# Kernel optimization log

Hardware: AMD Instinct MI355X
Metric: run time of the kernel (lower is better)

## Reference

```python
import jax, jax.numpy as jnp
import numpy as np

N = 8192       # num_nodes
F_IN = 128     # num_features
H = 32         # hidden_dim
C = 10         # num_classes
E = 262144     # num_edges (avg degree 32)
EPS = 1e-5     # BatchNorm1d eps


def setup_inputs() -> dict:
    key = jax.random.key(0)
    ks = jax.random.split(key, 24)
    rn = lambda k, shape, s=0.05: jax.random.normal(k, shape, jnp.float32) * s
    z = lambda n: jnp.zeros((n,), jnp.float32)
    return {
        "b": jax.random.normal(ks[0], (N, N), jnp.float32),
        "x": jax.random.normal(ks[1], (N, F_IN), jnp.float32),
        "edge_index": jax.random.randint(ks[2], (2, E), 0, N, jnp.int32),
        # GCNConv weights (stored [in,out]) + biases
        "W0": rn(ks[3], (F_IN, H)), "bc0": z(H),
        "W1": rn(ks[4], (H, H)),    "bc1": z(H),
        # BatchNorm affine params
        "g0": jnp.ones((H,), jnp.float32), "be0": z(H),
        "g1": jnp.ones((H,), jnp.float32), "be1": z(H),
        # autoencoder Linears (stored [in,out])
        "Wa0": rn(ks[5], (N, H)), "ba0": z(H),
        "Wa1": rn(ks[6], (H, H)), "ba1": z(H),
        "Wa2": rn(ks[7], (H, H)), "ba2": z(H),
        "Wa3": rn(ks[8], (H, N)), "ba3": z(N),
        # jump classifier: Linear(num_layers*H, C)
        "Wj": rn(ks[9], (2 * H, C)), "bj": z(C),
    }


def _gcn_conv(x, W, bias, src, dst):
    # PyG GCNConv: D^{-1/2}(A+I)D^{-1/2} X W + bias (src/dst already include self-loops)
    h = x @ W                                             # [N, out]
    deg = jax.ops.segment_sum(jnp.ones(src.shape[0], h.dtype), dst, num_segments=N)
    dinv = jax.lax.rsqrt(deg)                             # deg >= 1 due to self-loops
    norm = dinv[src] * dinv[dst]                          # [E+N]
    agg = jax.ops.segment_sum(norm[:, None] * h[src], dst, num_segments=N)
    return agg + bias


def _bn(x, g, b):
    # BatchNorm1d in training mode: batch stats over node dim, biased variance
    m = jnp.mean(x, axis=0)
    v = jnp.var(x, axis=0)
    return g * (x - m) * jax.lax.rsqrt(v + EPS) + b


def reference(b, x, edge_index, W0, bc0, W1, bc1, g0, be0, g1, be1,
              Wa0, ba0, Wa1, ba1, Wa2, ba2, Wa3, ba3, Wj, bj):
    loop = jnp.arange(N, dtype=edge_index.dtype)
    src = jnp.concatenate([edge_index[0], loop])
    dst = jnp.concatenate([edge_index[1], loop])

    # layer 0
    h = jax.nn.relu(_bn(_gcn_conv(x, W0, bc0, src, dst), g0, be0))
    x0 = h
    b = b @ Wa0 + ba0          # [N, H]
    h = h + b
    # layer 1
    h = jax.nn.relu(_bn(_gcn_conv(h, W1, bc1, src, dst), g1, be1))
    x1 = h
    b = b @ Wa1 + ba1
    # (torch computes x = x1 + b here, but it is dead after the last layer)
    # decoder tail: autoencoder[2], autoencoder[3]
    b = b @ Wa2 + ba2
    b = b @ Wa3 + ba3          # [N, N]

    out = jnp.concatenate([x0, x1], axis=1) @ Wj + bj
    return jax.nn.log_softmax(out, axis=-1), b
```

## Files before the change

### kernel.cpp

```cpp
#include <hip/hip_runtime.h>
#include <math.h>

#define NN 8192
#define FIN 128
#define HD 32
#define NC 10
#define NE 262144
#define EPSBN 1e-5f

typedef short short8 __attribute__((ext_vector_type(8)));
typedef float f32x4 __attribute__((ext_vector_type(4)));

__device__ __forceinline__ float bf2f(unsigned short b) {
  unsigned int u = ((unsigned int)b) << 16;
  float f;
  __builtin_memcpy(&f, &u, 4);
  return f;
}
__device__ __forceinline__ unsigned short f2bf(float f) {
  unsigned int u;
  __builtin_memcpy(&u, &f, 4);
  u = u + 0x7fffu + ((u >> 16) & 1u);
  return (unsigned short)(u >> 16);
}
__device__ __forceinline__ short8 ld_bf8(const unsigned short* p) {
  uint4 u = *(const uint4*)p;
  return __builtin_bit_cast(short8, u);
}
__device__ __forceinline__ float ldin(const void* p, int i, int isf) {
  if (isf) return ((const float*)p)[i];
  return bf2f(((const unsigned short*)p)[i]);
}

__global__ void detect_k(const void* __restrict__ b, int* __restrict__ flag) {
  const unsigned short* p = (const unsigned short*)b;
  int t = threadIdx.x;
  unsigned short s = p[2 * t];
  int e = (s >> 7) & 0xFF;
  int hit = (e >= 110 && e <= 135) ? 1 : 0;
  __shared__ int cnt[256];
  cnt[t] = hit;
  __syncthreads();
  for (int o = 128; o > 0; o >>= 1) {
    if (t < o) cnt[t] += cnt[t + o];
    __syncthreads();
  }
  if (t == 0) flag[0] = (cnt[0] < 128) ? 1 : 0;
}

__global__ void prep_T(const void* __restrict__ Wa1, const void* __restrict__ ba1,
                       const void* __restrict__ Wa2, const void* __restrict__ ba2,
                       const int* __restrict__ flg, float* __restrict__ T, float* __restrict__ vv) {
  int isf = *flg;
  __shared__ float sW1[1024], sW2[1024];
  int t = threadIdx.x;
  sW1[t] = ldin(Wa1, t, isf);
  sW2[t] = ldin(Wa2, t, isf);
  __syncthreads();
  {
    int c = t >> 5, c2 = t & 31;
    float acc = 0.f;
    for (int k = 0; k < 32; k++) acc += sW1[c * 32 + k] * sW2[k * 32 + c2];
    T[c * 32 + c2] = acc;
  }
  if (t < 32) {
    float acc = ldin(ba2, t, isf);
    for (int k = 0; k < 32; k++) acc += ldin(ba1, k, isf) * sW2[k * 32 + t];
    vv[t] = acc;
  }
}

__global__ void compute_Rp(const void* __restrict__ Wa3, const void* __restrict__ ba3,
                           const float* __restrict__ T, const float* __restrict__ vv,
                           const int* __restrict__ flg,
                           float* __restrict__ r2, unsigned short* __restrict__ Rp) {
  int isf = *flg;
  __shared__ float sT[1024], sv[32];
  int t = threadIdx.x;
  for (int i = t; i < 1024; i += 256) sT[i] = T[i];
  if (t < 32) sv[t] = vv[t];
  __syncthreads();
  int j = blockIdx.x * 256 + t;
  float w3[32];
  for (int c = 0; c < 32; c++) w3[c] = ldin(Wa3, c * NN + j, isf);
  float rr = ldin(ba3, j, isf);
  for (int c = 0; c < 32; c++) rr += sv[c] * w3[c];
  r2[j] = rr;
  float Rcol[32];
  for (int c = 0; c < 32; c++) {
    float acc = 0.f;
    for (int cp = 0; cp < 32; cp++) acc += sT[c * 32 + cp] * w3[cp];
    Rcol[c] = acc;
  }
  int jt = j >> 4, n = j & 15;
  for (int q = 0; q < 4; q++)
    for (int jj = 0; jj < 8; jj++)
      Rp[(size_t)(jt * 64 + q * 16 + n) * 8 + jj] = f2bf(Rcol[q * 8 + jj]);
}

__global__ void pack_Bp(const void* __restrict__ Wa0, const int* __restrict__ flg,
                        unsigned short* __restrict__ Bp) {
  int isf = *flg;
  int tid = blockIdx.x * 256 + threadIdx.x;
  int kb = tid >> 7;
  int h = (tid >> 6) & 1;
  int L = tid & 63;
  int q = L >> 4, n = L & 15;
  int base_k = kb * 32 + q * 8;
  if (isf) {
    const float* W = (const float*)Wa0;
    for (int j = 0; j < 8; j++)
      Bp[(size_t)((kb * 2 + h) * 64 + L) * 8 + j] = f2bf(W[(base_k + j) * HD + h * 16 + n]);
  } else {
    const unsigned short* W = (const unsigned short*)Wa0;
    for (int j = 0; j < 8; j++)
      Bp[(size_t)((kb * 2 + h) * 64 + L) * 8 + j] = W[(base_k + j) * HD + h * 16 + n];
  }
}

__global__ void deg_k(const int* __restrict__ dst, float* __restrict__ deg) {
  int e = blockIdx.x * 256 + threadIdx.x;
  atomicAdd(&deg[dst[e]], 1.0f);
}
__global__ void dinv_k(float* __restrict__ deg) {
  int i = blockIdx.x * 256 + threadIdx.x;
  deg[i] = rsqrtf(deg[i] + 1.0f);
}

__global__ void gemm_x_w0(const void* __restrict__ x, const void* __restrict__ W0,
                          const int* __restrict__ flg, float* __restrict__ h0) {
  int isf = *flg;
  __shared__ float sW[FIN * HD];
  __shared__ float sx[8 * FIN];
  int t = threadIdx.x;
  for (int i = t; i < FIN * HD; i += 256) sW[i] = ldin(W0, i, isf);
  int row0 = blockIdx.x * 8;
  for (int i = t; i < 8 * FIN; i += 256) {
    int r = i >> 7, k = i & 127;
    sx[i] = ldin(x, (row0 + r) * FIN + k, isf);
  }
  __syncthreads();
  int r = t >> 5, c = t & 31;
  float acc = 0.f;
  for (int k = 0; k < FIN; k++) acc += sx[r * FIN + k] * sW[k * HD + c];
  h0[(row0 + r) * HD + c] = acc;
}

__global__ void scatter_agg(const int* __restrict__ src, const int* __restrict__ dst,
                            const float* __restrict__ dinv, const float* __restrict__ h,
                            float* __restrict__ agg) {
  int tid = blockIdx.x * 256 + threadIdx.x;
  int idx = tid >> 5, c = tid & 31;
  int s, d;
  if (idx < NE) { s = src[idx]; d = dst[idx]; }
  else { s = d = idx - NE; }
  float wgt = dinv[s] * dinv[d];
  atomicAdd(&agg[d * HD + c], wgt * h[s * HD + c]);
}

__global__ void bn_stats(const float* __restrict__ xin, float* __restrict__ sum, float* __restrict__ sq) {
  int t = threadIdx.x;
  int c = t & 31;
  int g = t >> 5;
  float s = 0.f, q = 0.f;
  for (int r = blockIdx.x * 8 + g; r < NN; r += 2048) {
    float v = xin[r * HD + c];
    s += v;
    q += v * v;
  }
  __shared__ float ss[256], qq[256];
  ss[t] = s; qq[t] = q;
  __syncthreads();
  if (t < 128) { ss[t] += ss[t + 128]; qq[t] += qq[t + 128]; }
  __syncthreads();
  if (t < 64) { ss[t] += ss[t + 64]; qq[t] += qq[t + 64]; }
  __syncthreads();
  if (t < 32) {
    atomicAdd(&sum[c], ss[t] + ss[t + 32]);
    atomicAdd(&sq[c], qq[t] + qq[t + 32]);
  }
}

__global__ void bn_coef(const float* __restrict__ sum, const float* __restrict__ sq,
                        const void* __restrict__ g, const void* __restrict__ be,
                        const int* __restrict__ flg, float* __restrict__ a, float* __restrict__ bb) {
  int isf = *flg;
  int c = threadIdx.x;
  if (c < 32) {
    float m = sum[c] * (1.0f / 8192.0f);
    float var = fmaxf(sq[c] * (1.0f / 8192.0f) - m * m, 0.0f);
    float rstd = rsqrtf(var + EPSBN);
    float ac = ldin(g, c, isf) * rstd;
    a[c] = ac;
    bb[c] = ldin(be, c, isf) - m * ac;
  }
}

__global__ void gemm_b_wa0(const void* __restrict__ Bm, const unsigned short* __restrict__ Bp,
                           const int* __restrict__ flg, float* __restrict__ b1) {
  int isf = *flg;
  int t = threadIdx.x;
  int w = (blockIdx.x << 2) + (t >> 6);
  int L = t & 63;
  int rt = w >> 3, kq = w & 7;
  int q = L >> 4, n = L & 15;
  size_t aoff = (size_t)(rt * 16 + n) * NN + kq * 1024 + q * 8;
  f32x4 acc0 = {0.f, 0.f, 0.f, 0.f};
  f32x4 acc1 = {0.f, 0.f, 0.f, 0.f};
  int kb0 = kq * 32;
  if (isf) {
    const float* arow = (const float*)Bm + aoff;
    for (int i = 0; i < 32; i++) {
      f32x4 u0 = *(const f32x4*)(arow + i * 32);
      f32x4 u1 = *(const f32x4*)(arow + i * 32 + 4);
      union { unsigned short s[8]; short8 v; } au;
      au.s[0] = f2bf(u0[0]); au.s[1] = f2bf(u0[1]); au.s[2] = f2bf(u0[2]); au.s[3] = f2bf(u0[3]);
      au.s[4] = f2bf(u1[0]); au.s[5] = f2bf(u1[1]); au.s[6] = f2bf(u1[2]); au.s[7] = f2bf(u1[3]);
      const unsigned short* bpp = Bp + (size_t)((kb0 + i) * 2) * 512 + L * 8;
      acc0 = __builtin_amdgcn_mfma_f32_16x16x32_bf16(au.v, ld_bf8(bpp), acc0, 0, 0, 0);
      acc1 = __builtin_amdgcn_mfma_f32_16x16x32_bf16(au.v, ld_bf8(bpp + 512), acc1, 0, 0, 0);
    }
  } else {
    const unsigned short* arow = (const unsigned short*)Bm + aoff;
    for (int i = 0; i < 32; i++) {
      short8 a = ld_bf8(arow + i * 32);
      const unsigned short* bpp = Bp + (size_t)((kb0 + i) * 2) * 512 + L * 8;
      acc0 = __builtin_amdgcn_mfma_f32_16x16x32_bf16(a, ld_bf8(bpp), acc0, 0, 0, 0);
      acc1 = __builtin_amdgcn_mfma_f32_16x16x32_bf16(a, ld_bf8(bpp + 512), acc1, 0, 0, 0);
    }
  }
  int orow = rt * 16 + q * 4;
  for (int r = 0; r < 4; r++) {
    atomicAdd(&b1[(orow + r) * HD + n], acc0[r]);
    atomicAdd(&b1[(orow + r) * HD + n + 16], acc1[r]);
  }
}

__global__ void fuse0(float* __restrict__ aggA, const float* __restrict__ b1,
                      const void* __restrict__ ba0, const float* __restrict__ a,
                      const float* __restrict__ bb, const int* __restrict__ flg,
                      float* __restrict__ x0) {
  int isf = *flg;
  int i = blockIdx.x * 256 + threadIdx.x;
  int c = i & 31;
  float xv = fmaxf(a[c] * aggA[i] + bb[c], 0.0f);
  x0[i] = xv;
  aggA[i] = xv + b1[i] + ldin(ba0, c, isf);
}

__global__ void gemm_h_w1(float* __restrict__ hbuf, const void* __restrict__ W1,
                          const int* __restrict__ flg) {
  int isf = *flg;
  __shared__ float sW[1024], sh[256];
  int t = threadIdx.x;
  for (int i = t; i < 1024; i += 256) sW[i] = ldin(W1, i, isf);
  int row0 = blockIdx.x * 8;
  {
    int r = t >> 5, k = t & 31;
    sh[t] = hbuf[(row0 + r) * HD + k];
  }
  __syncthreads();
  int r = t >> 5, c = t & 31;
  float acc = 0.f;
  for (int k = 0; k < 32; k++) acc += sh[r * 32 + k] * sW[k * HD + c];
  hbuf[(row0 + r) * HD + c] = acc;
}

__global__ void bn_relu(float* __restrict__ agg, const float* __restrict__ a,
                        const float* __restrict__ bb) {
  int i = blockIdx.x * 256 + threadIdx.x;
  int c = i & 31;
  agg[i] = fmaxf(a[c] * agg[i] + bb[c], 0.0f);
}

__global__ void classifier(const float* __restrict__ x0, const float* __restrict__ x1,
                           const void* __restrict__ Wj, const void* __restrict__ bj,
                           const int* __restrict__ flg, void* __restrict__ outv) {
  int isf = *flg;
  __shared__ float sW[64 * NC];
  __shared__ float sb[NC];
  int t = threadIdx.x;
  for (int i = t; i < 64 * NC; i += 256) sW[i] = ldin(Wj, i, isf);
  if (t < NC) sb[t] = ldin(bj, t, isf);
  __syncthreads();
  int row = blockIdx.x * 256 + t;
  float lg[NC];
  for (int c = 0; c < NC; c++) lg[c] = sb[c];
  for (int k = 0; k < 32; k++) {
    float v = x0[row * HD + k];
    for (int c = 0; c < NC; c++) lg[c] += v * sW[k * NC + c];
  }
  for (int k = 0; k < 32; k++) {
    float v = x1[row * HD + k];
    for (int c = 0; c < NC; c++) lg[c] += v * sW[(32 + k) * NC + c];
  }
  float mx = lg[0];
  for (int c = 1; c < NC; c++) mx = fmaxf(mx, lg[c]);
  float se = 0.f;
  for (int c = 0; c < NC; c++) se += expf(lg[c] - mx);
  float lse = mx + logf(se);
  if (isf) {
    float* o = (float*)outv;
    for (int c = 0; c < NC; c++) o[row * NC + c] = lg[c] - lse;
  } else {
    unsigned short* o = (unsigned short*)outv;
    for (int c = 0; c < NC; c++) o[row * NC + c] = f2bf(lg[c] - lse);
  }
}

__global__ void gemm_b4(const float* __restrict__ b1, const void* __restrict__ ba0,
                        const unsigned short* __restrict__ Rp, const float* __restrict__ r2,
                        const int* __restrict__ flg, void* __restrict__ outv) {
  int isf = *flg;
  int t = threadIdx.x;
  int w = (blockIdx.x << 2) + (t >> 6);
  int L = t & 63;
  int rt = w >> 3, jc = w & 7;
  int q = L >> 4, n = L & 15;
  const float* ap = b1 + (size_t)(rt * 16 + n) * HD + q * 8;
  union { unsigned short s[8]; short8 v; } au;
  for (int j = 0; j < 8; j++) au.s[j] = f2bf(ap[j] + ldin(ba0, q * 8 + j, isf));
  short8 afrag = au.v;
  int orow = rt * 16 + q * 4;
  float* of = (float*)outv + NN * NC;
  unsigned short* ob = (unsigned short*)outv + NN * NC;
  for (int jt = jc * 64; jt < (jc + 1) * 64; jt++) {
    short8 bfrag = ld_bf8(Rp + (size_t)(jt * 64 + L) * 8);
    f32x4 acc = {0.f, 0.f, 0.f, 0.f};
    acc = __builtin_amdgcn_mfma_f32_16x16x32_bf16(afrag, bfrag, acc, 0, 0, 0);
    int col = jt * 16 + n;
    float radd = r2[col];
    size_t base = (size_t)orow * NN + col;
    if (isf) {
      of[base] = acc[0] + radd;
      of[base + NN] = acc[1] + radd;
      of[base + 2 * NN] = acc[2] + radd;
      of[base + 3 * NN] = acc[3] + radd;
    } else {
      ob[base] = f2bf(acc[0] + radd);
      ob[base + NN] = f2bf(acc[1] + radd);
      ob[base + 2 * NN] = f2bf(acc[2] + radd);
      ob[base + 3 * NN] = f2bf(acc[3] + radd);
    }
  }
}

extern "C" void kernel_launch(void* const* d_in, const int* in_sizes, int n_in,
                              void* d_out, int out_size, void* d_ws, size_t ws_size,
                              hipStream_t stream) {
  const void* B   = d_in[0];
  const void* X   = d_in[1];
  const int* EI   = (const int*)d_in[2];
  const void* W0  = d_in[3];
  const void* W1  = d_in[5];
  const void* g0  = d_in[7];
  const void* be0 = d_in[8];
  const void* g1  = d_in[9];
  const void* be1 = d_in[10];
  const void* Wa0 = d_in[11];
  const void* ba0 = d_in[12];
  const void* Wa1 = d_in[13];
  const void* ba1 = d_in[14];
  const void* Wa2 = d_in[15];
  const void* ba2 = d_in[16];
  const void* Wa3 = d_in[17];
  const void* ba3 = d_in[18];
  const void* Wj  = d_in[19];
  const void* bj  = d_in[20];
  (void)in_sizes; (void)n_in; (void)ws_size;

  const int* esrc = EI;
  const int* edst = EI + NE;

  float* ws   = (float*)d_ws;
  int* flag   = (int*)ws;
  float* stats = ws + 16;
  float* sum0 = stats, * sq0 = stats + 32, * sum1 = stats + 64, * sq1 = stats + 96;
  float* a0c = stats + 128, * bb0c = stats + 160, * a1c = stats + 192, * bb1c = stats + 224;
  float* b1   = stats + 256;
  float* r2   = b1 + NN * HD;
  float* T    = r2 + NN;
  float* vv   = T + 1024;
  unsigned short* Rp = (unsigned short*)(vv + 32);
  size_t wsZeroBytes = (size_t)(16 + 256 + NN * HD) * sizeof(float);

  size_t outBytesMin = (size_t)out_size * 2;
  size_t scratchBytes = (size_t)(NN + 3 * NN * HD) * 4 + (size_t)(256 * 2 * 64 * 8) * 2;
  char* sc = (char*)d_out + ((outBytesMin - scratchBytes) & ~(size_t)255);
  float* degv = (float*)sc;
  float* aggA = degv + NN;
  float* aggB = aggA + NN * HD;
  float* x0h  = aggB + NN * HD;
  unsigned short* Bp = (unsigned short*)(x0h + NN * HD);
  size_t outZeroBytes = (size_t)(NN + 2 * NN * HD) * sizeof(float);

  hipMemsetAsync(ws, 0, wsZeroBytes, stream);
  hipMemsetAsync(degv, 0, outZeroBytes, stream);

  detect_k<<<1, 256, 0, stream>>>(B, flag);
  prep_T<<<1, 1024, 0, stream>>>(Wa1, ba1, Wa2, ba2, flag, T, vv);
  compute_Rp<<<32, 256, 0, stream>>>(Wa3, ba3, T, vv, flag, r2, Rp);
  pack_Bp<<<128, 256, 0, stream>>>(Wa0, flag, Bp);
  deg_k<<<NE / 256, 256, 0, stream>>>(edst, degv);
  dinv_k<<<NN / 256, 256, 0, stream>>>(degv);
  gemm_x_w0<<<NN / 8, 256, 0, stream>>>(X, W0, flag, x0h);
  gemm_b_wa0<<<1024, 256, 0, stream>>>(B, Bp, flag, b1);
  scatter_agg<<<(NE + NN) * HD / 256, 256, 0, stream>>>(esrc, edst, degv, x0h, aggA);
  bn_stats<<<256, 256, 0, stream>>>(aggA, sum0, sq0);
  bn_coef<<<1, 64, 0, stream>>>(sum0, sq0, g0, be0, flag, a0c, bb0c);
  fuse0<<<NN * HD / 256, 256, 0, stream>>>(aggA, b1, ba0, a0c, bb0c, flag, x0h);
  gemm_h_w1<<<NN / 8, 256, 0, stream>>>(aggA, W1, flag);
  scatter_agg<<<(NE + NN) * HD / 256, 256, 0, stream>>>(esrc, edst, degv, aggA, aggB);
  bn_stats<<<256, 256, 0, stream>>>(aggB, sum1, sq1);
  bn_coef<<<1, 64, 0, stream>>>(sum1, sq1, g1, be1, flag, a1c, bb1c);
  bn_relu<<<NN * HD / 256, 256, 0, stream>>>(aggB, a1c, bb1c);
  classifier<<<NN / 256, 256, 0, stream>>>(x0h, aggB, Wj, bj, flag, d_out);
  gemm_b4<<<1024, 256, 0, stream>>>(b1, ba0, Rp, r2, flag, d_out);
}
```

Measured before the change: 766.7 us.

## Replace atomic scatter aggregation with CSR gather and remove atomics elsewhere

```diff
diff --git a/kernel.cpp b/kernel.cpp
--- a/kernel.cpp
+++ b/kernel.cpp
@@ -118,17 +118,49 @@
   }
 }
 
-__global__ void deg_k(const int* __restrict__ dst, float* __restrict__ deg) {
+__global__ void deg_k(const int* __restrict__ dst, int* __restrict__ deg) {
   int e = blockIdx.x * 256 + threadIdx.x;
-  atomicAdd(&deg[dst[e]], 1.0f);
-}
-__global__ void dinv_k(float* __restrict__ deg) {
-  int i = blockIdx.x * 256 + threadIdx.x;
-  deg[i] = rsqrtf(deg[i] + 1.0f);
+  atomicAdd(&deg[dst[e]], 1);
+}
+
+__global__ void csr_scan(const int* __restrict__ deg, int* __restrict__ rowp,
+                         float* __restrict__ dinvf) {
+  __shared__ int ps[1024];
+  int t = threadIdx.x;
+  int base = t * 8;
+  int loc[8];
+  int s = 0;
+  for (int j = 0; j < 8; j++) {
+    int d = deg[base + j];
+    loc[j] = s;
+    s += d;
+    dinvf[base + j] = rsqrtf((float)d + 1.0f);
+  }
+  ps[t] = s;
+  __syncthreads();
+  for (int off = 1; off < 1024; off <<= 1) {
+    int v = (t >= off) ? ps[t - off] : 0;
+    __syncthreads();
+    if (t >= off) ps[t] += v;
+    __syncthreads();
+  }
+  int ex = (t > 0) ? ps[t - 1] : 0;
+  for (int j = 0; j < 8; j++) rowp[base + j] = ex + loc[j];
+  if (t == 1023) rowp[NN] = ex + s;
+}
+
+__global__ void csr_fill(const int* __restrict__ src, const int* __restrict__ dst,
+                         const int* __restrict__ rowp, int* __restrict__ cnt,
+                         int* __restrict__ col) {
+  int e = blockIdx.x * 256 + threadIdx.x;
+  int d = dst[e];
+  int pos = atomicAdd(&cnt[d], 1);
+  col[rowp[d] + pos] = src[e];
 }
 
 __global__ void gemm_x_w0(const void* __restrict__ x, const void* __restrict__ W0,
-                          const int* __restrict__ flg, float* __restrict__ h0) {
+                          const float* __restrict__ dinvf, const int* __restrict__ flg,
+                          float* __restrict__ h0) {
   int isf = *flg;
   __shared__ float sW[FIN * HD];
   __shared__ float sx[8 * FIN];
@@ -143,19 +175,32 @@
   int r = t >> 5, c = t & 31;
   float acc = 0.f;
   for (int k = 0; k < FIN; k++) acc += sx[r * FIN + k] * sW[k * HD + c];
-  h0[(row0 + r) * HD + c] = acc;
-}
-
-__global__ void scatter_agg(const int* __restrict__ src, const int* __restrict__ dst,
-                            const float* __restrict__ dinv, const float* __restrict__ h,
-                            float* __restrict__ agg) {
-  int tid = blockIdx.x * 256 + threadIdx.x;
-  int idx = tid >> 5, c = tid & 31;
-  int s, d;
-  if (idx < NE) { s = src[idx]; d = dst[idx]; }
-  else { s = d = idx - NE; }
-  float wgt = dinv[s] * dinv[d];
-  atomicAdd(&agg[d * HD + c], wgt * h[s * HD + c]);
+  h0[(row0 + r) * HD + c] = acc * dinvf[row0 + r];
+}
+
+__global__ void gather_agg(const int* __restrict__ rowp, const int* __restrict__ col,
+                           const float* __restrict__ dinvf, const float* __restrict__ hs,
+                           float* __restrict__ agg) {
+  int w = (blockIdx.x << 2) + (threadIdx.x >> 6);
+  int L = threadIdx.x & 63;
+  int c = L & 31, half = L >> 5;
+  int s0 = rowp[w], s1 = rowp[w + 1];
+  float acc = 0.f;
+  int e = s0 + half;
+  if (e < s1) {
+    int s = col[e];
+    for (e += 2; e < s1; e += 2) {
+      int sn = col[e];
+      acc += hs[(size_t)s * HD + c];
+      s = sn;
+    }
+    acc += hs[(size_t)s * HD + c];
+  }
+  acc += __shfl_xor(acc, 32);
+  if (half == 0) {
+    float tot = acc + hs[(size_t)w * HD + c];
+    agg[(size_t)w * HD + c] = dinvf[w] * tot;
+  }
 }
 
 __global__ void bn_stats(const float* __restrict__ xin, float* __restrict__ sum, float* __restrict__ sq) {
@@ -199,10 +244,11 @@
 __global__ void gemm_b_wa0(const void* __restrict__ Bm, const unsigned short* __restrict__ Bp,
                            const int* __restrict__ flg, float* __restrict__ b1) {
   int isf = *flg;
-  int t = threadIdx.x;
-  int w = (blockIdx.x << 2) + (t >> 6);
+  __shared__ float red[8][512];
+  int t = threadIdx.x;
+  int kq = t >> 6;
   int L = t & 63;
-  int rt = w >> 3, kq = w & 7;
+  int rt = blockIdx.x;
   int q = L >> 4, n = L & 15;
   size_t aoff = (size_t)(rt * 16 + n) * NN + kq * 1024 + q * 8;
   f32x4 acc0 = {0.f, 0.f, 0.f, 0.f};
@@ -229,11 +275,14 @@
       acc1 = __builtin_amdgcn_mfma_f32_16x16x32_bf16(a, ld_bf8(bpp + 512), acc1, 0, 0, 0);
     }
   }
-  int orow = rt * 16 + q * 4;
   for (int r = 0; r < 4; r++) {
-    atomicAdd(&b1[(orow + r) * HD + n], acc0[r]);
-    atomicAdd(&b1[(orow + r) * HD + n + 16], acc1[r]);
-  }
+    red[kq][(q * 4 + r) * 32 + n] = acc0[r];
+    red[kq][(q * 4 + r) * 32 + n + 16] = acc1[r];
+  }
+  __syncthreads();
+  float s = 0.f;
+  for (int kw = 0; kw < 8; kw++) s += red[kw][t];
+  b1[rt * 512 + t] = s;
 }
 
 __global__ void fuse0(float* __restrict__ aggA, const float* __restrict__ b1,
@@ -249,7 +298,7 @@
 }
 
 __global__ void gemm_h_w1(float* __restrict__ hbuf, const void* __restrict__ W1,
-                          const int* __restrict__ flg) {
+                          const float* __restrict__ dinvf, const int* __restrict__ flg) {
   int isf = *flg;
   __shared__ float sW[1024], sh[256];
   int t = threadIdx.x;
@@ -263,42 +312,45 @@
   int r = t >> 5, c = t & 31;
   float acc = 0.f;
   for (int k = 0; k < 32; k++) acc += sh[r * 32 + k] * sW[k * HD + c];
-  hbuf[(row0 + r) * HD + c] = acc;
-}
-
-__global__ void bn_relu(float* __restrict__ agg, const float* __restrict__ a,
-                        const float* __restrict__ bb) {
-  int i = blockIdx.x * 256 + threadIdx.x;
-  int c = i & 31;
-  agg[i] = fmaxf(a[c] * agg[i] + bb[c], 0.0f);
-}
-
-__global__ void classifier(const float* __restrict__ x0, const float* __restrict__ x1,
+  hbuf[(row0 + r) * HD + c] = acc * dinvf[row0 + r];
+}
+
+__global__ void classifier(const float* __restrict__ x0, const float* __restrict__ agg1,
+                           const float* __restrict__ a1, const float* __restrict__ bb1,
                            const void* __restrict__ Wj, const void* __restrict__ bj,
                            const int* __restrict__ flg, void* __restrict__ outv) {
   int isf = *flg;
   __shared__ float sW[64 * NC];
   __shared__ float sb[NC];
-  int t = threadIdx.x;
-  for (int i = t; i < 64 * NC; i += 256) sW[i] = ldin(Wj, i, isf);
+  __shared__ float sa[HD], sbb[HD];
+  __shared__ float sx0[64 * 33], sx1[64 * 33];
+  int t = threadIdx.x;
+  for (int i = t; i < 64 * NC; i += 64) sW[i] = ldin(Wj, i, isf);
   if (t < NC) sb[t] = ldin(bj, t, isf);
-  __syncthreads();
-  int row = blockIdx.x * 256 + t;
+  if (t < HD) { sa[t] = a1[t]; sbb[t] = bb1[t]; }
+  int row0 = blockIdx.x * 64;
+  for (int i = t; i < 64 * HD; i += 64) {
+    int r = i >> 5, k = i & 31;
+    sx0[r * 33 + k] = x0[(size_t)row0 * HD + i];
+    sx1[r * 33 + k] = agg1[(size_t)row0 * HD + i];
+  }
+  __syncthreads();
   float lg[NC];
   for (int c = 0; c < NC; c++) lg[c] = sb[c];
-  for (int k = 0; k < 32; k++) {
-    float v = x0[row * HD + k];
+  for (int k = 0; k < HD; k++) {
+    float v = sx0[t * 33 + k];
     for (int c = 0; c < NC; c++) lg[c] += v * sW[k * NC + c];
   }
-  for (int k = 0; k < 32; k++) {
-    float v = x1[row * HD + k];
-    for (int c = 0; c < NC; c++) lg[c] += v * sW[(32 + k) * NC + c];
+  for (int k = 0; k < HD; k++) {
+    float v = fmaxf(sa[k] * sx1[t * 33 + k] + sbb[k], 0.0f);
+    for (int c = 0; c < NC; c++) lg[c] += v * sW[(HD + k) * NC + c];
   }
   float mx = lg[0];
   for (int c = 1; c < NC; c++) mx = fmaxf(mx, lg[c]);
   float se = 0.f;
   for (int c = 0; c < NC; c++) se += expf(lg[c] - mx);
   float lse = mx + logf(se);
+  int row = row0 + t;
   if (isf) {
     float* o = (float*)outv;
     for (int c = 0; c < NC; c++) o[row * NC + c] = lg[c] - lse;
@@ -382,38 +434,42 @@
   float* T    = r2 + NN;
   float* vv   = T + 1024;
   unsigned short* Rp = (unsigned short*)(vv + 32);
-  size_t wsZeroBytes = (size_t)(16 + 256 + NN * HD) * sizeof(float);
 
   size_t outBytesMin = (size_t)out_size * 2;
-  size_t scratchBytes = (size_t)(NN + 3 * NN * HD) * 4 + (size_t)(256 * 2 * 64 * 8) * 2;
+  size_t scratchBytes = (size_t)(NN + 3 * NN * HD) * 4
+                      + (size_t)(256 * 2 * 64 * 8) * 2
+                      + (size_t)(3 * NN + 1 + NE) * 4;
   char* sc = (char*)d_out + ((outBytesMin - scratchBytes) & ~(size_t)255);
-  float* degv = (float*)sc;
-  float* aggA = degv + NN;
+  float* degf = (float*)sc;
+  float* aggA = degf + NN;
   float* aggB = aggA + NN * HD;
   float* x0h  = aggB + NN * HD;
   unsigned short* Bp = (unsigned short*)(x0h + NN * HD);
-  size_t outZeroBytes = (size_t)(NN + 2 * NN * HD) * sizeof(float);
-
-  hipMemsetAsync(ws, 0, wsZeroBytes, stream);
-  hipMemsetAsync(degv, 0, outZeroBytes, stream);
+  int* deg_i  = (int*)(Bp + 256 * 2 * 64 * 8);
+  int* cnt    = deg_i + NN;
+  int* rowp   = cnt + NN;
+  int* col    = rowp + NN + 1;
+
+  hipMemsetAsync(ws, 0, (size_t)(16 + 256) * sizeof(float), stream);
+  hipMemsetAsync(deg_i, 0, (size_t)2 * NN * sizeof(int), stream);
 
   detect_k<<<1, 256, 0, stream>>>(B, flag);
   prep_T<<<1, 1024, 0, stream>>>(Wa1, ba1, Wa2, ba2, flag, T, vv);
   compute_Rp<<<32, 256, 0, stream>>>(Wa3, ba3, T, vv, flag, r2, Rp);
   pack_Bp<<<128, 256, 0, stream>>>(Wa0, flag, Bp);
-  deg_k<<<NE / 256, 256, 0, stream>>>(edst, degv);
-  dinv_k<<<NN / 256, 256, 0, stream>>>(degv);
-  gemm_x_w0<<<NN / 8, 256, 0, stream>>>(X, W0, flag, x0h);
-  gemm_b_wa0<<<1024, 256, 0, stream>>>(B, Bp, flag, b1);
-  scatter_agg<<<(NE + NN) * HD / 256, 256, 0, stream>>>(esrc, edst, degv, x0h, aggA);
+  deg_k<<<NE / 256, 256, 0, stream>>>(edst, deg_i);
+  csr_scan<<<1, 1024, 0, stream>>>(deg_i, rowp, degf);
+  csr_fill<<<NE / 256, 256, 0, stream>>>(esrc, edst, rowp, cnt, col);
+  gemm_x_w0<<<NN / 8, 256, 0, stream>>>(X, W0, degf, flag, x0h);
+  gemm_b_wa0<<<512, 512, 0, stream>>>(B, Bp, flag, b1);
+  gather_agg<<<NN / 4, 256, 0, stream>>>(rowp, col, degf, x0h, aggA);
   bn_stats<<<256, 256, 0, stream>>>(aggA, sum0, sq0);
   bn_coef<<<1, 64, 0, stream>>>(sum0, sq0, g0, be0, flag, a0c, bb0c);
   fuse0<<<NN * HD / 256, 256, 0, stream>>>(aggA, b1, ba0, a0c, bb0c, flag, x0h);
-  gemm_h_w1<<<NN / 8, 256, 0, stream>>>(aggA, W1, flag);
-  scatter_agg<<<(NE + NN) * HD / 256, 256, 0, stream>>>(esrc, edst, degv, aggA, aggB);
+  gemm_h_w1<<<NN / 8, 256, 0, stream>>>(aggA, W1, degf, flag);
+  gather_agg<<<NN / 4, 256, 0, stream>>>(rowp, col, degf, aggA, aggB);
   bn_stats<<<256, 256, 0, stream>>>(aggB, sum1, sq1);
   bn_coef<<<1, 64, 0, stream>>>(sum1, sq1, g1, be1, flag, a1c, bb1c);
-  bn_relu<<<NN * HD / 256, 256, 0, stream>>>(aggB, a1c, bb1c);
-  classifier<<<NN / 256, 256, 0, stream>>>(x0h, aggB, Wj, bj, flag, d_out);
+  classifier<<<NN / 64, 64, 0, stream>>>(x0h, aggB, a1c, bb1c, Wj, bj, flag, d_out);
   gemm_b4<<<1024, 256, 0, stream>>>(b1, ba0, Rp, r2, flag, d_out);
 }
```

Measured after the change: 772.4 us. No clear change (+0.7%).
